# Kernel optimization log

Measured on AMD Instinct MI355X. Metric: run time of the kernel, lower is better.

The kernel has to match this reference:

```python
import jax, jax.numpy as jnp
import numpy as np

N_HEADS = 16
EPS = 1e-12  # torch F.normalize eps


def srmsnorm(x):
    # F.normalize(x, dim=-1) * sqrt(dim)
    d = x.shape[-1]
    norm = jnp.sqrt(jnp.sum(x * x, axis=-1, keepdims=True))
    return x / jnp.maximum(norm, EPS) * jnp.sqrt(jnp.float32(d))


def setup_inputs() -> dict:
    key = jax.random.key(0)
    ks = jax.random.split(key, 7)
    B, S, D, F = 2, 2048, 1024, 4096
    x = jax.random.normal(ks[0], (B, S, D), dtype=jnp.float32)
    # xavier-uniform-ish scale for square weights
    lim = np.sqrt(6.0 / (D + D)).astype(np.float32)
    wq = jax.random.uniform(ks[1], (D, D), jnp.float32, -lim, lim)
    wk = jax.random.uniform(ks[2], (D, D), jnp.float32, -lim, lim)
    wv = jax.random.uniform(ks[3], (D, D), jnp.float32, -lim, lim)
    wo = jax.random.uniform(ks[4], (D, D), jnp.float32, -lim, lim)
    w_in = jax.random.normal(ks[5], (D, F), dtype=jnp.float32) * np.sqrt(2.0 / D).astype(np.float32)
    lim2 = np.sqrt(6.0 / (D + F)).astype(np.float32)
    w_out = jax.random.uniform(ks[6], (F, D), jnp.float32, -lim2, lim2)
    return {"x": x, "wq": wq, "wk": wk, "wv": wv, "wo": wo, "w_in": w_in, "w_out": w_out}


def attention(x, wq, wk, wv, wo):
    B, S, D = x.shape
    H = N_HEADS
    hd = D // H
    scale = hd ** -0.5
    q = (x @ wq).reshape(B, S, H, hd).transpose(0, 2, 1, 3)  # [B,H,S,hd]
    k = (x @ wk).reshape(B, S, H, hd).transpose(0, 2, 1, 3)
    v = (x @ wv).reshape(B, S, H, hd).transpose(0, 2, 1, 3)
    scores = jnp.einsum('bhqd,bhkd->bhqk', q, k) * scale  # [B,H,S,S]
    causal = jnp.tril(jnp.ones((S, S), dtype=bool))
    scores = jnp.where(causal, scores, jnp.float32(-jnp.inf))
    probs = jax.nn.softmax(scores, axis=-1)
    out = jnp.einsum('bhqk,bhkd->bhqd', probs, v)  # [B,H,S,hd]
    out = out.transpose(0, 2, 1, 3).reshape(B, S, D)
    return out @ wo


def reference(x, wq, wk, wv, wo, w_in, w_out):
    h = x + attention(srmsnorm(x), wq, wk, wv, wo)
    ff = jax.nn.gelu(srmsnorm(h) @ w_in, approximate=True) @ w_out
    return h + ff
```

## Files before the change

### kernel.cpp

```cpp
#include <hip/hip_runtime.h>
#include <math.h>

#define BB 2
#define SS 2048
#define DD 1024
#define FF 4096
#define HH 16
#define MM (BB * SS)

typedef __attribute__((ext_vector_type(8))) short short8v;
typedef __attribute__((ext_vector_type(4))) float float4v;
typedef __attribute__((ext_vector_type(4))) unsigned short ushort4v;
typedef __attribute__((ext_vector_type(8))) unsigned short ushort8v;
typedef unsigned short u16;
typedef unsigned int u32;

#define MFMA16(A_, B_, C_) __builtin_amdgcn_mfma_f32_16x16x32_bf16((A_), (B_), (C_), 0, 0, 0)

__device__ __forceinline__ u16 f2bf(float f) {
    u32 u = __float_as_uint(f);
    u += 0x7FFF + ((u >> 16) & 1);
    return (u16)(u >> 16);
}

__device__ __forceinline__ void async16(void* lds, const void* g) {
    __builtin_amdgcn_global_load_lds(
        (const __attribute__((address_space(1))) u32*)g,
        (__attribute__((address_space(3))) u32*)lds, 16, 0, 0);
}

__device__ __forceinline__ float gelu_f(float x) {
    float u = 0.7978845608028654f * x * (1.0f + 0.044715f * x * x);
    float e = exp2f(u * 2.8853900817779268f);
    float th = 1.0f - 2.0f / (e + 1.0f);
    return 0.5f * x * (1.0f + th);
}

__global__ __launch_bounds__(256) void srmsnorm_bf16(const float* __restrict__ in,
                                                     u16* __restrict__ out) {
    const int row = blockIdx.x, t = threadIdx.x;
    float4 a = reinterpret_cast<const float4*>(in + (size_t)row * DD)[t];
    float ss = a.x * a.x + a.y * a.y + a.z * a.z + a.w * a.w;
#pragma unroll
    for (int off = 32; off > 0; off >>= 1) ss += __shfl_xor(ss, off);
    __shared__ float red[4];
    if ((t & 63) == 0) red[t >> 6] = ss;
    __syncthreads();
    float tot = red[0] + red[1] + red[2] + red[3];
    float sc = 32.0f / fmaxf(sqrtf(tot), 1e-12f);
    ushort4v ov;
    ov[0] = f2bf(a.x * sc); ov[1] = f2bf(a.y * sc);
    ov[2] = f2bf(a.z * sc); ov[3] = f2bf(a.w * sc);
    *(ushort4v*)(out + (size_t)row * DD + t * 4) = ov;
}

__global__ __launch_bounds__(256) void wtrans(const float* __restrict__ in,
                                              u16* __restrict__ out, int K, int N) {
    __shared__ float T[64][65];
    const int t = threadIdx.x;
    const int n0 = blockIdx.x * 64, k0 = blockIdx.y * 64;
#pragma unroll
    for (int i = 0; i < 4; ++i) {
        int r = i * 16 + (t >> 4), c4 = (t & 15) * 4;
        float4 v = *reinterpret_cast<const float4*>(in + (size_t)(k0 + r) * N + n0 + c4);
        T[r][c4 + 0] = v.x; T[r][c4 + 1] = v.y; T[r][c4 + 2] = v.z; T[r][c4 + 3] = v.w;
    }
    __syncthreads();
#pragma unroll
    for (int i = 0; i < 4; ++i) {
        int r = i * 16 + (t >> 4), c4 = (t & 15) * 4;
        ushort4v ov;
#pragma unroll
        for (int j = 0; j < 4; ++j) ov[j] = f2bf(T[c4 + j][r]);
        *(ushort4v*)(out + (size_t)(n0 + r) * K + k0 + c4) = ov;
    }
}

__global__ __launch_bounds__(256) void vtrans(const u16* __restrict__ vb,
                                              u16* __restrict__ vt) {
    __shared__ u16 T[64][88];
    const int t = threadIdx.x;
    const int s0 = blockIdx.x * 64, bh = blockIdx.y;
    const int b = bh >> 4, h = bh & 15;
#pragma unroll
    for (int i = 0; i < 2; ++i) {
        int r = i * 32 + (t >> 3), c8 = (t & 7) * 8;
        *(ushort8v*)&T[r][c8] =
            *(const ushort8v*)(vb + (size_t)(b * SS + s0 + r) * DD + h * 64 + c8);
    }
    __syncthreads();
#pragma unroll
    for (int i = 0; i < 2; ++i) {
        int d = i * 32 + (t >> 3), s8 = (t & 7) * 8;
        ushort8v ov;
#pragma unroll
        for (int j = 0; j < 8; ++j) ov[j] = T[s8 + j][d];
        *(ushort8v*)(vt + ((size_t)bh * 64 + d) * SS + s0 + s8) = ov;
    }
}

template <int BM, int BN, int EPI>
__global__ __launch_bounds__(256) void gemm_bf16(const u16* __restrict__ A,
                                                 const u16* __restrict__ Bt,
                                                 const float* __restrict__ Res,
                                                 void* __restrict__ Cout,
                                                 int M, int N, int K) {
    __shared__ u16 As[BM * 32];
    __shared__ u16 Bs[BN * 32];
    constexpr int FM = BM / 32, FN = BN / 32;
    const int t = threadIdx.x;
    const int w = t >> 6, lane = t & 63;
    const int g = lane >> 4, c = lane & 15;
    const int wr = w >> 1, wc = w & 1;
    const int bm = blockIdx.y * BM, bn = blockIdx.x * BN;
    const int arow = t >> 2, au = (t & 3) * 8;

    float4v acc[FM][FN] = {};
    for (int k0 = 0; k0 < K; k0 += 32) {
        __syncthreads();
#pragma unroll
        for (int p = 0; p < BM / 64; ++p)
            async16(&As[(p * 64 + arow) * 32 + au],
                    A + (size_t)(bm + p * 64 + arow) * K + k0 + au);
#pragma unroll
        for (int p = 0; p < BN / 64; ++p)
            async16(&Bs[(p * 64 + arow) * 32 + au],
                    Bt + (size_t)(bn + p * 64 + arow) * K + k0 + au);
        __syncthreads();
        short8v af[FM], bf[FN];
#pragma unroll
        for (int mi = 0; mi < FM; ++mi)
            af[mi] = *(const short8v*)&As[(wr * (BM / 2) + mi * 16 + c) * 32 + g * 8];
#pragma unroll
        for (int ni = 0; ni < FN; ++ni)
            bf[ni] = *(const short8v*)&Bs[(wc * (BN / 2) + ni * 16 + c) * 32 + g * 8];
#pragma unroll
        for (int mi = 0; mi < FM; ++mi)
#pragma unroll
            for (int ni = 0; ni < FN; ++ni)
                acc[mi][ni] = MFMA16(af[mi], bf[ni], acc[mi][ni]);
    }
    const int row0 = bm + wr * (BM / 2), col0 = bn + wc * (BN / 2);
#pragma unroll
    for (int mi = 0; mi < FM; ++mi)
#pragma unroll
        for (int r = 0; r < 4; ++r) {
            const size_t rw = (size_t)(row0 + mi * 16 + 4 * g + r) * N;
#pragma unroll
            for (int ni = 0; ni < FN; ++ni) {
                const size_t off = rw + col0 + ni * 16 + c;
                float v = acc[mi][ni][r];
                if (EPI == 0)      ((u16*)Cout)[off] = f2bf(v);
                else if (EPI == 1) ((float*)Cout)[off] = v + Res[off];
                else               ((u16*)Cout)[off] = f2bf(gelu_f(v));
            }
        }
}

__global__ __launch_bounds__(256) void attn_mfma(const u16* __restrict__ Qb,
                                                 const u16* __restrict__ Kb,
                                                 const u16* __restrict__ Vt,
                                                 u16* __restrict__ Ao) {
    __shared__ u16 Pl[4][2][16][88];
    const int t = threadIdx.x;
    const int w = t >> 6, lane = t & 63;
    const int g = lane >> 4, c = lane & 15;
    const int bh = blockIdx.x;
    const int qt = (int)(gridDim.y - 1) - (int)blockIdx.y;
    const int b = bh >> 4, h = bh & 15;
    const int qrow0 = qt * 128 + w * 32;
    const int ktmax = (qrow0 + 31) >> 6;
    const size_t qkbase = (size_t)b * SS * DD + h * 64;
    const size_t vbase = (size_t)bh * 64 * SS;
    constexpr float SC = 0.18033688011112042f;

    short8v qf[2][2];
#pragma unroll
    for (int rb = 0; rb < 2; ++rb)
#pragma unroll
        for (int kh = 0; kh < 2; ++kh)
            qf[rb][kh] = *(const short8v*)(Qb + qkbase +
                             (size_t)(qrow0 + rb * 16 + c) * DD + kh * 32 + g * 8);

    float4v o[2][4] = {};
    float m_run[2][4], l_run[2][4];
#pragma unroll
    for (int rb = 0; rb < 2; ++rb)
#pragma unroll
        for (int r = 0; r < 4; ++r) { m_run[rb][r] = -1e30f; l_run[rb][r] = 0.0f; }

    for (int kt = 0; kt <= ktmax; ++kt) {
        short8v kf[4][2];
#pragma unroll
        for (int nb = 0; nb < 4; ++nb)
#pragma unroll
            for (int kh = 0; kh < 2; ++kh)
                kf[nb][kh] = *(const short8v*)(Kb + qkbase +
                                 (size_t)(kt * 64 + nb * 16 + c) * DD + kh * 32 + g * 8);
        float4v sa[2][4] = {};
#pragma unroll
        for (int nb = 0; nb < 4; ++nb)
#pragma unroll
            for (int kh = 0; kh < 2; ++kh)
#pragma unroll
                for (int rb = 0; rb < 2; ++rb)
                    sa[rb][nb] = MFMA16(qf[rb][kh], kf[nb][kh], sa[rb][nb]);

        const bool diag = (kt == ktmax);
#pragma unroll
        for (int rb = 0; rb < 2; ++rb)
#pragma unroll
            for (int nb = 0; nb < 4; ++nb)
#pragma unroll
                for (int r = 0; r < 4; ++r) {
                    float v = sa[rb][nb][r] * SC;
                    if (diag && (kt * 64 + nb * 16 + c > qrow0 + rb * 16 + 4 * g + r))
                        v = -3e38f;
                    sa[rb][nb][r] = v;
                }

#pragma unroll
        for (int rb = 0; rb < 2; ++rb) {
            float mx[4], corr[4];
#pragma unroll
            for (int r = 0; r < 4; ++r) {
                float m0 = fmaxf(fmaxf(sa[rb][0][r], sa[rb][1][r]),
                                 fmaxf(sa[rb][2][r], sa[rb][3][r]));
                m0 = fmaxf(m0, __shfl_xor(m0, 1));
                m0 = fmaxf(m0, __shfl_xor(m0, 2));
                m0 = fmaxf(m0, __shfl_xor(m0, 4));
                m0 = fmaxf(m0, __shfl_xor(m0, 8));
                float mn = fmaxf(m_run[rb][r], m0);
                corr[r] = exp2f(m_run[rb][r] - mn);
                m_run[rb][r] = mn;
                mx[r] = mn;
            }
#pragma unroll
            for (int nb = 0; nb < 4; ++nb)
#pragma unroll
                for (int r = 0; r < 4; ++r)
                    sa[rb][nb][r] = exp2f(sa[rb][nb][r] - mx[r]);
#pragma unroll
            for (int r = 0; r < 4; ++r) {
                float s_ = sa[rb][0][r] + sa[rb][1][r] + sa[rb][2][r] + sa[rb][3][r];
                s_ += __shfl_xor(s_, 1); s_ += __shfl_xor(s_, 2);
                s_ += __shfl_xor(s_, 4); s_ += __shfl_xor(s_, 8);
                l_run[rb][r] = l_run[rb][r] * corr[r] + s_;
            }
            float4v cv; cv[0] = corr[0]; cv[1] = corr[1]; cv[2] = corr[2]; cv[3] = corr[3];
#pragma unroll
            for (int nb = 0; nb < 4; ++nb) o[rb][nb] *= cv;
#pragma unroll
            for (int nb = 0; nb < 4; ++nb)
#pragma unroll
                for (int r = 0; r < 4; ++r)
                    Pl[w][rb][4 * g + r][nb * 16 + c] = f2bf(sa[rb][nb][r]);
        }

        short8v pa[2][2];
#pragma unroll
        for (int rb = 0; rb < 2; ++rb)
#pragma unroll
            for (int kh = 0; kh < 2; ++kh)
                pa[rb][kh] = *(const short8v*)&Pl[w][rb][c][kh * 32 + g * 8];
        short8v vf[4][2];
#pragma unroll
        for (int nb = 0; nb < 4; ++nb)
#pragma unroll
            for (int kh = 0; kh < 2; ++kh)
                vf[nb][kh] = *(const short8v*)(Vt + vbase +
                                 (size_t)(nb * 16 + c) * SS + kt * 64 + kh * 32 + g * 8);
#pragma unroll
        for (int nb = 0; nb < 4; ++nb)
#pragma unroll
            for (int kh = 0; kh < 2; ++kh)
#pragma unroll
                for (int rb = 0; rb < 2; ++rb)
                    o[rb][nb] = MFMA16(pa[rb][kh], vf[nb][kh], o[rb][nb]);
    }

#pragma unroll
    for (int rb = 0; rb < 2; ++rb) {
        float inv[4];
#pragma unroll
        for (int r = 0; r < 4; ++r) inv[r] = 1.0f / l_run[rb][r];
#pragma unroll
        for (int nb = 0; nb < 4; ++nb)
#pragma unroll
            for (int r = 0; r < 4; ++r)
                Ao[qkbase + (size_t)(qrow0 + rb * 16 + 4 * g + r) * DD + nb * 16 + c] =
                    f2bf(o[rb][nb][r] * inv[r]);
    }
}

extern "C" void kernel_launch(void* const* d_in, const int* in_sizes, int n_in,
                              void* d_out, int out_size, void* d_ws, size_t ws_size,
                              hipStream_t stream) {
    const float* x     = (const float*)d_in[0];
    const float* wq    = (const float*)d_in[1];
    const float* wk    = (const float*)d_in[2];
    const float* wv    = (const float*)d_in[3];
    const float* wo    = (const float*)d_in[4];
    const float* w_in  = (const float*)d_in[5];
    const float* w_out = (const float*)d_in[6];
    float* out = (float*)d_out;
    char* ws = (char*)d_ws;
    const size_t MB = 1024 * 1024;
    u16* wq_t  = (u16*)(ws + 0 * MB);
    u16* wk_t  = (u16*)(ws + 2 * MB);
    u16* wv_t  = (u16*)(ws + 4 * MB);
    u16* wo_t  = (u16*)(ws + 6 * MB);
    u16* wi_t  = (u16*)(ws + 8 * MB);
    u16* wo2_t = (u16*)(ws + 16 * MB);
    u16* xn    = (u16*)(ws + 24 * MB);
    u16* qb    = (u16*)(ws + 32 * MB);
    u16* kb    = (u16*)(ws + 40 * MB);
    u16* vb    = (u16*)(ws + 48 * MB);
    u16* vt    = (u16*)(ws + 56 * MB);
    u16* ao    = (u16*)(ws + 64 * MB);
    u16* hn    = (u16*)(ws + 72 * MB);
    u16* gbuf  = (u16*)(ws + 80 * MB);

    dim3 blk(256);
    wtrans<<<dim3(DD / 64, DD / 64), blk, 0, stream>>>(wq, wq_t, DD, DD);
    wtrans<<<dim3(DD / 64, DD / 64), blk, 0, stream>>>(wk, wk_t, DD, DD);
    wtrans<<<dim3(DD / 64, DD / 64), blk, 0, stream>>>(wv, wv_t, DD, DD);
    wtrans<<<dim3(DD / 64, DD / 64), blk, 0, stream>>>(wo, wo_t, DD, DD);
    wtrans<<<dim3(FF / 64, DD / 64), blk, 0, stream>>>(w_in, wi_t, DD, FF);
    wtrans<<<dim3(DD / 64, FF / 64), blk, 0, stream>>>(w_out, wo2_t, FF, DD);

    srmsnorm_bf16<<<MM, blk, 0, stream>>>(x, xn);
    gemm_bf16<128, 64, 0><<<dim3(DD / 64, MM / 128), blk, 0, stream>>>(xn, wq_t, nullptr, qb, MM, DD, DD);
    gemm_bf16<128, 64, 0><<<dim3(DD / 64, MM / 128), blk, 0, stream>>>(xn, wk_t, nullptr, kb, MM, DD, DD);
    gemm_bf16<128, 64, 0><<<dim3(DD / 64, MM / 128), blk, 0, stream>>>(xn, wv_t, nullptr, vb, MM, DD, DD);
    vtrans<<<dim3(SS / 64, BB * HH), blk, 0, stream>>>(vb, vt);
    attn_mfma<<<dim3(BB * HH, SS / 128), blk, 0, stream>>>(qb, kb, vt, ao);
    gemm_bf16<128, 64, 1><<<dim3(DD / 64, MM / 128), blk, 0, stream>>>(ao, wo_t, x, out, MM, DD, DD);
    srmsnorm_bf16<<<MM, blk, 0, stream>>>(out, hn);
    gemm_bf16<128, 128, 2><<<dim3(FF / 128, MM / 128), blk, 0, stream>>>(hn, wi_t, nullptr, gbuf, MM, FF, DD);
    gemm_bf16<128, 64, 1><<<dim3(DD / 64, MM / 128), blk, 0, stream>>>(gbuf, wo2_t, out, out, MM, DD, FF);
}
```

Before: 459.4 us.

## Fuse QKV projections into one GEMM and shrink attention blocks to one wave

The three Q/K/V projection GEMMs become a single N=3072 GEMM. A new epilogue scatters each 1024-column segment into separate contiguous buffers, relying on wq_t, wk_t and wv_t sitting back-to-back in the workspace. The attention kernel now runs one 64-thread wave per 16 query rows in a flat grid, ordered heaviest tiles first, to improve causal load balance and occupancy, at the cost of more redundant K/V reads. The output-projection and FFN-down GEMMs also move to 128x128 tiles.

```diff
diff --git a/kernel.cpp b/kernel.cpp
--- a/kernel.cpp
+++ b/kernel.cpp
@@ -141,6 +141,20 @@
                 acc[mi][ni] = MFMA16(af[mi], bf[ni], acc[mi][ni]);
     }
     const int row0 = bm + wr * (BM / 2), col0 = bn + wc * (BN / 2);
+    if (EPI == 3) {
+        const int seg = col0 >> 10, c0 = col0 & 1023;
+        u16* dst = (u16*)Cout + (size_t)seg * ((size_t)MM * 1024);
+#pragma unroll
+        for (int mi = 0; mi < FM; ++mi)
+#pragma unroll
+            for (int r = 0; r < 4; ++r) {
+                const size_t rw = (size_t)(row0 + mi * 16 + 4 * g + r) * 1024;
+#pragma unroll
+                for (int ni = 0; ni < FN; ++ni)
+                    dst[rw + c0 + ni * 16 + c] = f2bf(acc[mi][ni][r]);
+            }
+        return;
+    }
 #pragma unroll
     for (int mi = 0; mi < FM; ++mi)
 #pragma unroll
@@ -157,37 +171,32 @@
         }
 }
 
-__global__ __launch_bounds__(256) void attn_mfma(const u16* __restrict__ Qb,
-                                                 const u16* __restrict__ Kb,
-                                                 const u16* __restrict__ Vt,
-                                                 u16* __restrict__ Ao) {
-    __shared__ u16 Pl[4][2][16][88];
-    const int t = threadIdx.x;
-    const int w = t >> 6, lane = t & 63;
+__global__ __launch_bounds__(64) void attn_mfma(const u16* __restrict__ Qb,
+                                                const u16* __restrict__ Kb,
+                                                const u16* __restrict__ Vt,
+                                                u16* __restrict__ Ao) {
+    __shared__ u16 Pl[16][88];
+    const int lane = threadIdx.x;
     const int g = lane >> 4, c = lane & 15;
-    const int bh = blockIdx.x;
-    const int qt = (int)(gridDim.y - 1) - (int)blockIdx.y;
+    const int bid = blockIdx.x;
+    const int bh = bid & 31;
+    const int u = 127 - (bid >> 5);
     const int b = bh >> 4, h = bh & 15;
-    const int qrow0 = qt * 128 + w * 32;
-    const int ktmax = (qrow0 + 31) >> 6;
+    const int qrow0 = u * 16;
+    const int ktmax = qrow0 >> 6;
     const size_t qkbase = (size_t)b * SS * DD + h * 64;
     const size_t vbase = (size_t)bh * 64 * SS;
     constexpr float SC = 0.18033688011112042f;
 
-    short8v qf[2][2];
-#pragma unroll
-    for (int rb = 0; rb < 2; ++rb)
-#pragma unroll
-        for (int kh = 0; kh < 2; ++kh)
-            qf[rb][kh] = *(const short8v*)(Qb + qkbase +
-                             (size_t)(qrow0 + rb * 16 + c) * DD + kh * 32 + g * 8);
-
-    float4v o[2][4] = {};
-    float m_run[2][4], l_run[2][4];
-#pragma unroll
-    for (int rb = 0; rb < 2; ++rb)
-#pragma unroll
-        for (int r = 0; r < 4; ++r) { m_run[rb][r] = -1e30f; l_run[rb][r] = 0.0f; }
+    short8v qf[2];
+#pragma unroll
+    for (int kh = 0; kh < 2; ++kh)
+        qf[kh] = *(const short8v*)(Qb + qkbase +
+                     (size_t)(qrow0 + c) * DD + kh * 32 + g * 8);
+
+    float4v o[4] = {};
+    float m_run[4] = {-1e30f, -1e30f, -1e30f, -1e30f};
+    float l_run[4] = {0.0f, 0.0f, 0.0f, 0.0f};
 
     for (int kt = 0; kt <= ktmax; ++kt) {
         short8v kf[4][2];
@@ -197,72 +206,62 @@
             for (int kh = 0; kh < 2; ++kh)
                 kf[nb][kh] = *(const short8v*)(Kb + qkbase +
                                  (size_t)(kt * 64 + nb * 16 + c) * DD + kh * 32 + g * 8);
-        float4v sa[2][4] = {};
+        float4v sa[4] = {};
 #pragma unroll
         for (int nb = 0; nb < 4; ++nb)
 #pragma unroll
             for (int kh = 0; kh < 2; ++kh)
-#pragma unroll
-                for (int rb = 0; rb < 2; ++rb)
-                    sa[rb][nb] = MFMA16(qf[rb][kh], kf[nb][kh], sa[rb][nb]);
+                sa[nb] = MFMA16(qf[kh], kf[nb][kh], sa[nb]);
 
         const bool diag = (kt == ktmax);
 #pragma unroll
-        for (int rb = 0; rb < 2; ++rb)
-#pragma unroll
-            for (int nb = 0; nb < 4; ++nb)
-#pragma unroll
-                for (int r = 0; r < 4; ++r) {
-                    float v = sa[rb][nb][r] * SC;
-                    if (diag && (kt * 64 + nb * 16 + c > qrow0 + rb * 16 + 4 * g + r))
-                        v = -3e38f;
-                    sa[rb][nb][r] = v;
-                }
-
-#pragma unroll
-        for (int rb = 0; rb < 2; ++rb) {
-            float mx[4], corr[4];
+        for (int nb = 0; nb < 4; ++nb)
 #pragma unroll
             for (int r = 0; r < 4; ++r) {
-                float m0 = fmaxf(fmaxf(sa[rb][0][r], sa[rb][1][r]),
-                                 fmaxf(sa[rb][2][r], sa[rb][3][r]));
-                m0 = fmaxf(m0, __shfl_xor(m0, 1));
-                m0 = fmaxf(m0, __shfl_xor(m0, 2));
-                m0 = fmaxf(m0, __shfl_xor(m0, 4));
-                m0 = fmaxf(m0, __shfl_xor(m0, 8));
-                float mn = fmaxf(m_run[rb][r], m0);
-                corr[r] = exp2f(m_run[rb][r] - mn);
-                m_run[rb][r] = mn;
-                mx[r] = mn;
+                float v = sa[nb][r] * SC;
+                if (diag && (kt * 64 + nb * 16 + c > qrow0 + 4 * g + r))
+                    v = -3e38f;
+                sa[nb][r] = v;
             }
-#pragma unroll
-            for (int nb = 0; nb < 4; ++nb)
-#pragma unroll
-                for (int r = 0; r < 4; ++r)
-                    sa[rb][nb][r] = exp2f(sa[rb][nb][r] - mx[r]);
-#pragma unroll
-            for (int r = 0; r < 4; ++r) {
-                float s_ = sa[rb][0][r] + sa[rb][1][r] + sa[rb][2][r] + sa[rb][3][r];
-                s_ += __shfl_xor(s_, 1); s_ += __shfl_xor(s_, 2);
-                s_ += __shfl_xor(s_, 4); s_ += __shfl_xor(s_, 8);
-                l_run[rb][r] = l_run[rb][r] * corr[r] + s_;
-            }
-            float4v cv; cv[0] = corr[0]; cv[1] = corr[1]; cv[2] = corr[2]; cv[3] = corr[3];
-#pragma unroll
-            for (int nb = 0; nb < 4; ++nb) o[rb][nb] *= cv;
-#pragma unroll
-            for (int nb = 0; nb < 4; ++nb)
-#pragma unroll
-                for (int r = 0; r < 4; ++r)
-                    Pl[w][rb][4 * g + r][nb * 16 + c] = f2bf(sa[rb][nb][r]);
+
+        float corr[4];
+#pragma unroll
+        for (int r = 0; r < 4; ++r) {
+            float m0 = fmaxf(fmaxf(sa[0][r], sa[1][r]), fmaxf(sa[2][r], sa[3][r]));
+            m0 = fmaxf(m0, __shfl_xor(m0, 1));
+            m0 = fmaxf(m0, __shfl_xor(m0, 2));
+            m0 = fmaxf(m0, __shfl_xor(m0, 4));
+            m0 = fmaxf(m0, __shfl_xor(m0, 8));
+            float mn = fmaxf(m_run[r], m0);
+            corr[r] = exp2f(m_run[r] - mn);
+            m_run[r] = mn;
         }
-
-        short8v pa[2][2];
-#pragma unroll
-        for (int rb = 0; rb < 2; ++rb)
-#pragma unroll
-            for (int kh = 0; kh < 2; ++kh)
-                pa[rb][kh] = *(const short8v*)&Pl[w][rb][c][kh * 32 + g * 8];
+#pragma unroll
+        for (int nb = 0; nb < 4; ++nb)
+#pragma unroll
+            for (int r = 0; r < 4; ++r)
+                sa[nb][r] = exp2f(sa[nb][r] - m_run[r]);
+#pragma unroll
+        for (int r = 0; r < 4; ++r) {
+            float s_ = sa[0][r] + sa[1][r] + sa[2][r] + sa[3][r];
+            s_ += __shfl_xor(s_, 1); s_ += __shfl_xor(s_, 2);
+            s_ += __shfl_xor(s_, 4); s_ += __shfl_xor(s_, 8);
+            l_run[r] = l_run[r] * corr[r] + s_;
+        }
+        float4v cv; cv[0] = corr[0]; cv[1] = corr[1]; cv[2] = corr[2]; cv[3] = corr[3];
+#pragma unroll
+        for (int nb = 0; nb < 4; ++nb) o[nb] *= cv;
+
+#pragma unroll
+        for (int nb = 0; nb < 4; ++nb)
+#pragma unroll
+            for (int r = 0; r < 4; ++r)
+                Pl[4 * g + r][nb * 16 + c] = f2bf(sa[nb][r]);
+
+        short8v pa[2];
+#pragma unroll
+        for (int kh = 0; kh < 2; ++kh)
+            pa[kh] = *(const short8v*)&Pl[c][kh * 32 + g * 8];
         short8v vf[4][2];
 #pragma unroll
         for (int nb = 0; nb < 4; ++nb)
@@ -274,23 +273,18 @@
         for (int nb = 0; nb < 4; ++nb)
 #pragma unroll
             for (int kh = 0; kh < 2; ++kh)
-#pragma unroll
-                for (int rb = 0; rb < 2; ++rb)
-                    o[rb][nb] = MFMA16(pa[rb][kh], vf[nb][kh], o[rb][nb]);
-    }
-
-#pragma unroll
-    for (int rb = 0; rb < 2; ++rb) {
-        float inv[4];
-#pragma unroll
-        for (int r = 0; r < 4; ++r) inv[r] = 1.0f / l_run[rb][r];
-#pragma unroll
-        for (int nb = 0; nb < 4; ++nb)
-#pragma unroll
-            for (int r = 0; r < 4; ++r)
-                Ao[qkbase + (size_t)(qrow0 + rb * 16 + 4 * g + r) * DD + nb * 16 + c] =
-                    f2bf(o[rb][nb][r] * inv[r]);
-    }
+                o[nb] = MFMA16(pa[kh], vf[nb][kh], o[nb]);
+    }
+
+    float inv[4];
+#pragma unroll
+    for (int r = 0; r < 4; ++r) inv[r] = 1.0f / l_run[r];
+#pragma unroll
+    for (int nb = 0; nb < 4; ++nb)
+#pragma unroll
+        for (int r = 0; r < 4; ++r)
+            Ao[qkbase + (size_t)(qrow0 + 4 * g + r) * DD + nb * 16 + c] =
+                f2bf(o[nb][r] * inv[r]);
 }
 
 extern "C" void kernel_launch(void* const* d_in, const int* in_sizes, int n_in,
@@ -314,7 +308,6 @@
     u16* wo2_t = (u16*)(ws + 16 * MB);
     u16* xn    = (u16*)(ws + 24 * MB);
     u16* qb    = (u16*)(ws + 32 * MB);
-    u16* kb    = (u16*)(ws + 40 * MB);
     u16* vb    = (u16*)(ws + 48 * MB);
     u16* vt    = (u16*)(ws + 56 * MB);
     u16* ao    = (u16*)(ws + 64 * MB);
@@ -330,13 +323,12 @@
     wtrans<<<dim3(DD / 64, FF / 64), blk, 0, stream>>>(w_out, wo2_t, FF, DD);
 
     srmsnorm_bf16<<<MM, blk, 0, stream>>>(x, xn);
-    gemm_bf16<128, 64, 0><<<dim3(DD / 64, MM / 128), blk, 0, stream>>>(xn, wq_t, nullptr, qb, MM, DD, DD);
-    gemm_bf16<128, 64, 0><<<dim3(DD / 64, MM / 128), blk, 0, stream>>>(xn, wk_t, nullptr, kb, MM, DD, DD);
-    gemm_bf16<128, 64, 0><<<dim3(DD / 64, MM / 128), blk, 0, stream>>>(xn, wv_t, nullptr, vb, MM, DD, DD);
+    gemm_bf16<128, 128, 3><<<dim3(3072 / 128, MM / 128), blk, 0, stream>>>(
+        xn, wq_t, nullptr, qb, MM, 3072, DD);
     vtrans<<<dim3(SS / 64, BB * HH), blk, 0, stream>>>(vb, vt);
-    attn_mfma<<<dim3(BB * HH, SS / 128), blk, 0, stream>>>(qb, kb, vt, ao);
-    gemm_bf16<128, 64, 1><<<dim3(DD / 64, MM / 128), blk, 0, stream>>>(ao, wo_t, x, out, MM, DD, DD);
+    attn_mfma<<<dim3(32 * 128), dim3(64), 0, stream>>>(qb, qb + (size_t)MM * 1024, vt, ao);
+    gemm_bf16<128, 128, 1><<<dim3(DD / 128, MM / 128), blk, 0, stream>>>(ao, wo_t, x, out, MM, DD, DD);
     srmsnorm_bf16<<<MM, blk, 0, stream>>>(out, hn);
     gemm_bf16<128, 128, 2><<<dim3(FF / 128, MM / 128), blk, 0, stream>>>(hn, wi_t, nullptr, gbuf, MM, FF, DD);
-    gemm_bf16<128, 64, 1><<<dim3(DD / 64, MM / 128), blk, 0, stream>>>(gbuf, wo2_t, out, out, MM, DD, FF);
-}
+    gemm_bf16<128, 128, 1><<<dim3(DD / 128, MM / 128), blk, 0, stream>>>(gbuf, wo2_t, out, out, MM, DD, FF);
+}
```

New measurement: 467.4 us. Within noise of the previous version (+1.7%).
